# Performance work log

Hardware: AMD Instinct MI355X
Metric: run time of the kernel (lower is better)

The kernel has to match this reference:

```python
import jax, jax.numpy as jnp
import numpy as np
from math import exp

WINDOW_SIZE = 11
CHANNEL = 3
DATA_RANGE = 1.0
K1 = 0.01
K2 = 0.03


def _create_window(window_size=WINDOW_SIZE, channel=CHANNEL, sigma=1.5):
    g = np.array([exp(-(x - window_size // 2) ** 2 / float(2 * sigma ** 2))
                  for x in range(window_size)], dtype=np.float32)
    g = g / g.sum()
    w2d = np.outer(g, g).astype(np.float32)  # (k, k)
    # depthwise kernel, OIHW with I=1, O=channel
    return jnp.asarray(np.broadcast_to(w2d, (channel, 1, window_size, window_size)).copy())


def _depthwise_conv(x, window):
    pad = WINDOW_SIZE // 2
    return jax.lax.conv_general_dilated(
        x, window, window_strides=(1, 1),
        padding=[(pad, pad), (pad, pad)],
        dimension_numbers=('NCHW', 'OIHW', 'NCHW'),
        feature_group_count=CHANNEL)


def setup_inputs() -> dict:
    key = jax.random.key(0)
    k1, k2 = jax.random.split(key)
    img1 = jax.random.uniform(k1, (32, 3, 512, 512), dtype=jnp.float32)
    img2 = jax.random.uniform(k2, (32, 3, 512, 512), dtype=jnp.float32)
    return {"img1": img1, "img2": img2}


def reference(img1, img2):
    window = _create_window()
    mu1 = _depthwise_conv(img1, window)
    mu2 = _depthwise_conv(img2, window)
    mu1_sq = mu1 * mu1
    mu2_sq = mu2 * mu2
    mu1_mu2 = mu1 * mu2
    sigma1_sq = jnp.clip(_depthwise_conv(img1 * img1, window) - mu1_sq, 0.0, None)
    sigma2_sq = jnp.clip(_depthwise_conv(img2 * img2, window) - mu2_sq, 0.0, None)
    sigma12 = _depthwise_conv(img1 * img2, window) - mu1_mu2
    C1 = (K1 * DATA_RANGE) ** 2
    C2 = (K2 * DATA_RANGE) ** 2
    ssim_map = ((2 * mu1_mu2 + C1) * (2 * sigma12 + C2)) / ((mu1_sq + mu2_sq + C1) * (sigma1_sq + sigma2_sq + C2))
    return 1.0 - ssim_map.mean()
```

## Files before the change

### kernel.cpp

```cpp
#include <hip/hip_runtime.h>

typedef float v2f __attribute__((ext_vector_type(2)));

#define W_IMG 512
#define H_IMG 512
#define PLANES 96
#define NPIX 25165824.0

#define SWIDE 128
#define SH 64
#define NROWS (SH + 10)
#define NQUAD 36
#define NPRS  72
#define XS (W_IMG / SWIDE)
#define YB (H_IMG / SH)
#define WPB 2

__global__ void ssim_zero(double* acc) {
    const int t = threadIdx.x;
    if (t < PLANES) acc[t] = 0.0;
}

__global__ void ssim_final(const double* __restrict__ acc, float* __restrict__ out) {
    const int L = threadIdx.x;
    double s = (L < PLANES) ? acc[L] : 0.0;
    if (L + 64 < PLANES) s += acc[L + 64];
    #pragma unroll
    for (int off = 32; off > 0; off >>= 1) s += __shfl_down(s, off, 64);
    if (L == 0) out[0] = (float)(1.0 - s / NPIX);
}

__device__ __forceinline__ v2f pk_add2(v2f a, v2f b) {
    v2f d; asm("v_pk_add_f32 %0, %1, %2" : "=v"(d) : "v"(a), "v"(b)); return d;
}
__device__ __forceinline__ v2f pk_mul2(v2f a, v2f b) {
    v2f d; asm("v_pk_mul_f32 %0, %1, %2" : "=v"(d) : "v"(a), "v"(b)); return d;
}
__device__ __forceinline__ v2f pk_fma2(v2f a, v2f b, v2f c) {
    asm("v_pk_fma_f32 %0, %1, %2, %0" : "+v"(c) : "v"(a), "v"(b)); return c;
}

__global__ __launch_bounds__(128, 2)
void ssim_main(const float* __restrict__ img1,
               const float* __restrict__ img2,
               double* __restrict__ acc)
{
    constexpr float G0=0.00102838f, G1=0.00759875f, G2c=0.03600077f,
                    G3=0.10936070f, G4=0.21300540f, G5=0.26601180f,
                    G6=0.21300540f, G7=0.10936070f, G8=0.03600077f,
                    G9=0.00759875f, G10=0.00102838f;
    constexpr float K_C1 = 0.0001f;
    constexpr float K_C2 = 0.0009f;

    const v2f Gp1[6] = { {0.f,G0}, {G1,G2c}, {G3,G4}, {G5,G6}, {G7,G8}, {G9,G10} };
    const v2f Gp2[6] = { {G0,G1}, {G2c,G3}, {G4,G5}, {G6,G7}, {G8,G9}, {G10,0.f} };
    const v2f GV[11] = { {G0,G0},{G1,G1},{G2c,G2c},{G3,G3},{G4,G4},{G5,G5},
                         {G6,G6},{G7,G7},{G8,G8},{G9,G9},{G10,G10} };

    __shared__ __align__(16) float4 sp[WPB][2][NPRS];

    const int tid = threadIdx.x;
    const int wv  = tid >> 6;
    const int L   = tid & 63;
    const int wid = blockIdx.x * WPB + wv;
    const int c0  = (wid & (XS - 1)) * SWIDE;
    const int r0  = (wid >> 2) * SH;
    const int plane = blockIdx.y;
    const size_t pofs = (size_t)plane * (H_IMG * W_IMG);
    const float* __restrict__ p1 = img1 + pofs;
    const float* __restrict__ p2 = img2 + pofs;

    const int gq  = c0 - 8 + 4 * L;
    const bool qok = (L < NQUAD) && (gq >= 0) && (gq <= W_IMG - 4);
    const bool sth = (L < NQUAD);

    float4 qa = make_float4(0.f,0.f,0.f,0.f), qb = qa;
    auto LOADROW = [&](int s) {
        qa = make_float4(0.f,0.f,0.f,0.f); qb = qa;
        const int gr = r0 - 5 + s;
        if (qok && (unsigned)gr < (unsigned)H_IMG) {
            const int off = gr * W_IMG + gq;
            __builtin_memcpy(&qa, p1 + off, 16);
            __builtin_memcpy(&qb, p2 + off, 16);
        }
    };
    auto STORE = [&](int buf) {
        if (sth) {
            sp[wv][buf][2*L]   = make_float4(qa.x, qa.y, qb.x, qb.y);
            sp[wv][buf][2*L+1] = make_float4(qa.z, qa.w, qb.z, qb.w);
        }
    };

    v2f ring_m1[11], ring_m2[11], ring_ab[11], ring_s2[11];
    float lsum = 0.f;
    const v2f z2 = {0.f, 0.f};

    LOADROW(0); STORE(0); LOADROW(1);

    int cur = 0;
    #pragma unroll 1
    for (int sb = 0; sb < 77; sb += 11) {
        #pragma unroll
        for (int j = 0; j < 11; ++j) {
            const int s = sb + j;

            if (s + 1 < NROWS) STORE(cur ^ 1);
            if (s + 2 < NROWS) LOADROW(s + 2);

            if (s < NROWS) {
                v2f m1a=z2, m2a=z2, aba=z2, s2a=z2;
                v2f m1b=z2, m2b=z2, abb=z2, s2b=z2;
                #pragma unroll
                for (int p = 0; p < 7; ++p) {
                    const float4 P = sp[wv][cur][L + 1 + p];
                    const v2f ap = {P.x, P.y};
                    const v2f bp = {P.z, P.w};
                    const v2f spp = pk_add2(ap, bp);
                    if (p < 6) {
                        const v2f g = Gp1[p];
                        m1a = pk_fma2(g, ap, m1a);
                        m2a = pk_fma2(g, bp, m2a);
                        const v2f t1 = pk_mul2(g, ap);
                        aba = pk_fma2(t1, bp, aba);
                        const v2f t2 = pk_mul2(g, spp);
                        s2a = pk_fma2(t2, spp, s2a);
                    }
                    if (p > 0) {
                        const v2f g = Gp2[p - 1];
                        m1b = pk_fma2(g, ap, m1b);
                        m2b = pk_fma2(g, bp, m2b);
                        const v2f t1 = pk_mul2(g, ap);
                        abb = pk_fma2(t1, bp, abb);
                        const v2f t2 = pk_mul2(g, spp);
                        s2b = pk_fma2(t2, spp, s2b);
                    }
                }
                ring_m1[j] = (v2f){ m1a.x + m1a.y, m1b.x + m1b.y };
                ring_m2[j] = (v2f){ m2a.x + m2a.y, m2b.x + m2b.y };
                ring_ab[j] = (v2f){ aba.x + aba.y, abb.x + abb.y };
                ring_s2[j] = (v2f){ s2a.x + s2a.y, s2b.x + s2b.y };
            }

            if (s >= 10 && s < NROWS) {
                v2f M1=z2, M2=z2, AB=z2, S2=z2;
                #pragma unroll
                for (int k = 0; k < 11; ++k) {
                    const int sl = (j + 1 + k) % 11;
                    M1 = pk_fma2(GV[k], ring_m1[sl], M1);
                    M2 = pk_fma2(GV[k], ring_m2[sl], M2);
                    AB = pk_fma2(GV[k], ring_ab[sl], AB);
                    S2 = pk_fma2(GV[k], ring_s2[sl], S2);
                }
                #pragma unroll
                for (int h = 0; h < 2; ++h) {
                    const float u1 = h ? M1.y : M1.x;
                    const float u2 = h ? M2.y : M2.x;
                    const float eab = h ? AB.y : AB.x;
                    const float es2 = h ? S2.y : S2.x;
                    const float mu12 = u1 * u2;
                    const float musq = fmaf(u1, u1, u2 * u2);
                    const float sig12 = eab - mu12;
                    const float sigsum = fmaxf(fmaf(-2.f, eab, es2) - musq, 0.f);
                    const float num = fmaf(2.f, mu12, K_C1) * fmaf(2.f, sig12, K_C2);
                    const float den = (musq + K_C1) * (sigsum + K_C2);
                    lsum = fmaf(num, __builtin_amdgcn_rcpf(den), lsum);
                }
            }

            cur ^= 1;
        }
    }

    #pragma unroll
    for (int off = 32; off > 0; off >>= 1)
        lsum += __shfl_down(lsum, off, 64);
    if (L == 0)
        atomicAdd(&acc[plane], (double)lsum);
}

extern "C" void kernel_launch(void* const* d_in, const int* in_sizes, int n_in,
                              void* d_out, int out_size, void* d_ws, size_t ws_size,
                              hipStream_t stream) {
    const float* img1 = (const float*)d_in[0];
    const float* img2 = (const float*)d_in[1];
    float* out  = (float*)d_out;
    double* acc = (double*)d_ws;

    ssim_zero<<<dim3(1), dim3(128), 0, stream>>>(acc);
    ssim_main<<<dim3(XS * YB / WPB, PLANES), dim3(64 * WPB), 0, stream>>>(img1, img2, acc);
    ssim_final<<<dim3(1), dim3(64), 0, stream>>>(acc, out);
}
```

Measured before the change: 115.7 us.

## Use fp16 dot2 horizontal convolution with one output column per lane

```diff
diff --git a/kernel.cpp b/kernel.cpp
--- a/kernel.cpp
+++ b/kernel.cpp
@@ -1,24 +1,23 @@
 #include <hip/hip_runtime.h>
 
-typedef float v2f __attribute__((ext_vector_type(2)));
+typedef __fp16 h2 __attribute__((ext_vector_type(2)));
 
 #define W_IMG 512
 #define H_IMG 512
 #define PLANES 96
 #define NPIX 25165824.0
 
-#define SWIDE 128
-#define SH 64
+#define SW 64
+#define SH 32
 #define NROWS (SH + 10)
-#define NQUAD 36
-#define NPRS  72
-#define XS (W_IMG / SWIDE)
+#define NSLOT 20
+#define WPB 4
+#define XS (W_IMG / SW)
 #define YB (H_IMG / SH)
-#define WPB 2
+#define BPP (XS * YB / WPB)
 
 __global__ void ssim_zero(double* acc) {
-    const int t = threadIdx.x;
-    if (t < PLANES) acc[t] = 0.0;
+    if (threadIdx.x < PLANES) acc[threadIdx.x] = 0.0;
 }
 
 __global__ void ssim_final(const double* __restrict__ acc, float* __restrict__ out) {
@@ -30,53 +29,61 @@
     if (L == 0) out[0] = (float)(1.0 - s / NPIX);
 }
 
-__device__ __forceinline__ v2f pk_add2(v2f a, v2f b) {
-    v2f d; asm("v_pk_add_f32 %0, %1, %2" : "=v"(d) : "v"(a), "v"(b)); return d;
-}
-__device__ __forceinline__ v2f pk_mul2(v2f a, v2f b) {
-    v2f d; asm("v_pk_mul_f32 %0, %1, %2" : "=v"(d) : "v"(a), "v"(b)); return d;
-}
-__device__ __forceinline__ v2f pk_fma2(v2f a, v2f b, v2f c) {
-    asm("v_pk_fma_f32 %0, %1, %2, %0" : "+v"(c) : "v"(a), "v"(b)); return c;
+__device__ __forceinline__ float dot2(h2 a, h2 b, float c) {
+    asm("v_dot2_f32_f16 %0, %1, %2, %0" : "+v"(c) : "v"(a), "v"(b));
+    return c;
 }
 
-__global__ __launch_bounds__(128, 2)
+union HU { h2 h; unsigned u; };
+
+__global__ __launch_bounds__(256, 2)
 void ssim_main(const float* __restrict__ img1,
                const float* __restrict__ img2,
                double* __restrict__ acc)
 {
-    constexpr float G0=0.00102838f, G1=0.00759875f, G2c=0.03600077f,
-                    G3=0.10936070f, G4=0.21300540f, G5=0.26601180f,
-                    G6=0.21300540f, G7=0.10936070f, G8=0.03600077f,
-                    G9=0.00759875f, G10=0.00102838f;
+    constexpr float G[11] = {
+        0.00102838f, 0.00759875f, 0.03600077f, 0.10936070f, 0.21300540f,
+        0.26601180f,
+        0.21300540f, 0.10936070f, 0.03600077f, 0.00759875f, 0.00102838f };
     constexpr float K_C1 = 0.0001f;
     constexpr float K_C2 = 0.0009f;
 
-    const v2f Gp1[6] = { {0.f,G0}, {G1,G2c}, {G3,G4}, {G5,G6}, {G7,G8}, {G9,G10} };
-    const v2f Gp2[6] = { {G0,G1}, {G2c,G3}, {G4,G5}, {G6,G7}, {G8,G9}, {G10,0.f} };
-    const v2f GV[11] = { {G0,G0},{G1,G1},{G2c,G2c},{G3,G3},{G4,G4},{G5,G5},
-                         {G6,G6},{G7,G7},{G8,G8},{G9,G9},{G10,G10} };
-
-    __shared__ __align__(16) float4 sp[WPB][2][NPRS];
+    __shared__ __align__(16) uint4 sbuf[WPB][2][NSLOT];
 
     const int tid = threadIdx.x;
     const int wv  = tid >> 6;
     const int L   = tid & 63;
     const int wid = blockIdx.x * WPB + wv;
-    const int c0  = (wid & (XS - 1)) * SWIDE;
-    const int r0  = (wid >> 2) * SH;
+    const int c0  = (wid & (XS - 1)) * SW;
+    const int r0  = (wid >> 3) * SH;
     const int plane = blockIdx.y;
     const size_t pofs = (size_t)plane * (H_IMG * W_IMG);
     const float* __restrict__ p1 = img1 + pofs;
     const float* __restrict__ p2 = img2 + pofs;
 
+    const int sh = (L + 3) & 3;
+    const int s0 = (L + 3) >> 2;
+    h2 gs[8];
+    #pragma unroll
+    for (int m = 0; m < 16; m += 2) {
+        float lo = 0.f, hi = 0.f;
+        #pragma unroll
+        for (int t = 0; t < 11; ++t) {
+            lo = (m     - sh == t) ? G[t] : lo;
+            hi = (m + 1 - sh == t) ? G[t] : hi;
+        }
+        gs[m >> 1] = __builtin_amdgcn_cvt_pkrtz(lo, hi);
+    }
+
+    const uint4* __restrict__ bp0 = &sbuf[wv][0][s0];
+    const uint4* __restrict__ bp1 = &sbuf[wv][1][s0];
+
     const int gq  = c0 - 8 + 4 * L;
-    const bool qok = (L < NQUAD) && (gq >= 0) && (gq <= W_IMG - 4);
-    const bool sth = (L < NQUAD);
+    const bool qok = (L < NSLOT) && (gq >= 0) && (gq <= W_IMG - 4);
+    float4 qa = make_float4(0.f, 0.f, 0.f, 0.f), qb = qa;
 
-    float4 qa = make_float4(0.f,0.f,0.f,0.f), qb = qa;
     auto LOADROW = [&](int s) {
-        qa = make_float4(0.f,0.f,0.f,0.f); qb = qa;
+        qa = make_float4(0.f, 0.f, 0.f, 0.f); qb = qa;
         const int gr = r0 - 5 + s;
         if (qok && (unsigned)gr < (unsigned)H_IMG) {
             const int off = gr * W_IMG + gq;
@@ -85,89 +92,81 @@
         }
     };
     auto STORE = [&](int buf) {
-        if (sth) {
-            sp[wv][buf][2*L]   = make_float4(qa.x, qa.y, qb.x, qb.y);
-            sp[wv][buf][2*L+1] = make_float4(qa.z, qa.w, qb.z, qb.w);
+        if (L < NSLOT) {
+            HU a0, a1, b0, b1;
+            a0.h = __builtin_amdgcn_cvt_pkrtz(qa.x, qa.y);
+            a1.h = __builtin_amdgcn_cvt_pkrtz(qa.z, qa.w);
+            b0.h = __builtin_amdgcn_cvt_pkrtz(qb.x, qb.y);
+            b1.h = __builtin_amdgcn_cvt_pkrtz(qb.z, qb.w);
+            sbuf[wv][buf][L] = make_uint4(a0.u, a1.u, b0.u, b1.u);
         }
     };
 
-    v2f ring_m1[11], ring_m2[11], ring_ab[11], ring_s2[11];
+    float rM1[11], rM2[11], rEA[11], rEB[11], rEAB[11];
     float lsum = 0.f;
-    const v2f z2 = {0.f, 0.f};
 
     LOADROW(0); STORE(0); LOADROW(1);
 
-    int cur = 0;
     #pragma unroll 1
-    for (int sb = 0; sb < 77; sb += 11) {
+    for (int sb = 0; sb < 44; sb += 22) {
         #pragma unroll
-        for (int j = 0; j < 11; ++j) {
+        for (int j = 0; j < 22; ++j) {
             const int s = sb + j;
 
-            if (s + 1 < NROWS) STORE(cur ^ 1);
+            if (s + 1 < NROWS) STORE((j + 1) & 1);
             if (s + 2 < NROWS) LOADROW(s + 2);
 
             if (s < NROWS) {
-                v2f m1a=z2, m2a=z2, aba=z2, s2a=z2;
-                v2f m1b=z2, m2b=z2, abb=z2, s2b=z2;
+                const uint4* bp = ((j & 1) == 0) ? bp0 : bp1;
+                const uint4 w0 = bp[0], w1 = bp[1], w2 = bp[2], w3 = bp[3];
+                h2 av[8], bv[8];
+                {
+                    HU t;
+                    t.u = w0.x; av[0] = t.h;  t.u = w0.y; av[1] = t.h;
+                    t.u = w0.z; bv[0] = t.h;  t.u = w0.w; bv[1] = t.h;
+                    t.u = w1.x; av[2] = t.h;  t.u = w1.y; av[3] = t.h;
+                    t.u = w1.z; bv[2] = t.h;  t.u = w1.w; bv[3] = t.h;
+                    t.u = w2.x; av[4] = t.h;  t.u = w2.y; av[5] = t.h;
+                    t.u = w2.z; bv[4] = t.h;  t.u = w2.w; bv[5] = t.h;
+                    t.u = w3.x; av[6] = t.h;  t.u = w3.y; av[7] = t.h;
+                    t.u = w3.z; bv[6] = t.h;  t.u = w3.w; bv[7] = t.h;
+                }
+                float m1 = 0.f, m2 = 0.f, ea = 0.f, eb = 0.f, eab = 0.f;
                 #pragma unroll
-                for (int p = 0; p < 7; ++p) {
-                    const float4 P = sp[wv][cur][L + 1 + p];
-                    const v2f ap = {P.x, P.y};
-                    const v2f bp = {P.z, P.w};
-                    const v2f spp = pk_add2(ap, bp);
-                    if (p < 6) {
-                        const v2f g = Gp1[p];
-                        m1a = pk_fma2(g, ap, m1a);
-                        m2a = pk_fma2(g, bp, m2a);
-                        const v2f t1 = pk_mul2(g, ap);
-                        aba = pk_fma2(t1, bp, aba);
-                        const v2f t2 = pk_mul2(g, spp);
-                        s2a = pk_fma2(t2, spp, s2a);
-                    }
-                    if (p > 0) {
-                        const v2f g = Gp2[p - 1];
-                        m1b = pk_fma2(g, ap, m1b);
-                        m2b = pk_fma2(g, bp, m2b);
-                        const v2f t1 = pk_mul2(g, ap);
-                        abb = pk_fma2(t1, bp, abb);
-                        const v2f t2 = pk_mul2(g, spp);
-                        s2b = pk_fma2(t2, spp, s2b);
-                    }
+                for (int p = 0; p < 8; ++p) {
+                    m1 = dot2(gs[p], av[p], m1);
+                    m2 = dot2(gs[p], bv[p], m2);
+                    const h2 w  = gs[p] * av[p];
+                    const h2 ww = gs[p] * bv[p];
+                    ea  = dot2(w,  av[p], ea);
+                    eab = dot2(w,  bv[p], eab);
+                    eb  = dot2(ww, bv[p], eb);
                 }
-                ring_m1[j] = (v2f){ m1a.x + m1a.y, m1b.x + m1b.y };
-                ring_m2[j] = (v2f){ m2a.x + m2a.y, m2b.x + m2b.y };
-                ring_ab[j] = (v2f){ aba.x + aba.y, abb.x + abb.y };
-                ring_s2[j] = (v2f){ s2a.x + s2a.y, s2b.x + s2b.y };
+                const int sl = (j < 11) ? j : j - 11;
+                rM1[sl] = m1;  rM2[sl] = m2;
+                rEA[sl] = ea;  rEB[sl] = eb;  rEAB[sl] = eab;
             }
 
             if (s >= 10 && s < NROWS) {
-                v2f M1=z2, M2=z2, AB=z2, S2=z2;
+                float M1 = 0.f, M2 = 0.f, EA = 0.f, EB = 0.f, EAB = 0.f;
                 #pragma unroll
                 for (int k = 0; k < 11; ++k) {
                     const int sl = (j + 1 + k) % 11;
-                    M1 = pk_fma2(GV[k], ring_m1[sl], M1);
-                    M2 = pk_fma2(GV[k], ring_m2[sl], M2);
-                    AB = pk_fma2(GV[k], ring_ab[sl], AB);
-                    S2 = pk_fma2(GV[k], ring_s2[sl], S2);
+                    M1  = fmaf(G[k], rM1[sl],  M1);
+                    M2  = fmaf(G[k], rM2[sl],  M2);
+                    EA  = fmaf(G[k], rEA[sl],  EA);
+                    EB  = fmaf(G[k], rEB[sl],  EB);
+                    EAB = fmaf(G[k], rEAB[sl], EAB);
                 }
-                #pragma unroll
-                for (int h = 0; h < 2; ++h) {
-                    const float u1 = h ? M1.y : M1.x;
-                    const float u2 = h ? M2.y : M2.x;
-                    const float eab = h ? AB.y : AB.x;
-                    const float es2 = h ? S2.y : S2.x;
-                    const float mu12 = u1 * u2;
-                    const float musq = fmaf(u1, u1, u2 * u2);
-                    const float sig12 = eab - mu12;
-                    const float sigsum = fmaxf(fmaf(-2.f, eab, es2) - musq, 0.f);
-                    const float num = fmaf(2.f, mu12, K_C1) * fmaf(2.f, sig12, K_C2);
-                    const float den = (musq + K_C1) * (sigsum + K_C2);
-                    lsum = fmaf(num, __builtin_amdgcn_rcpf(den), lsum);
-                }
+                const float mu12 = M1 * M2;
+                const float mu1s = M1 * M1, mu2s = M2 * M2;
+                const float v11 = fmaxf(EA - mu1s, 0.f);
+                const float v22 = fmaxf(EB - mu2s, 0.f);
+                const float v12 = EAB - mu12;
+                const float num = fmaf(2.f, mu12, K_C1) * fmaf(2.f, v12, K_C2);
+                const float den = (mu1s + mu2s + K_C1) * (v11 + v22 + K_C2);
+                lsum = fmaf(num, __builtin_amdgcn_rcpf(den), lsum);
             }
-
-            cur ^= 1;
         }
     }
 
@@ -187,6 +186,6 @@
     double* acc = (double*)d_ws;
 
     ssim_zero<<<dim3(1), dim3(128), 0, stream>>>(acc);
-    ssim_main<<<dim3(XS * YB / WPB, PLANES), dim3(64 * WPB), 0, stream>>>(img1, img2, acc);
+    ssim_main<<<dim3(BPP, PLANES), dim3(256), 0, stream>>>(img1, img2, acc);
     ssim_final<<<dim3(1), dim3(64), 0, stream>>>(acc, out);
 }
```

New measurement: 145.9 us. 26.1% more time.
